# Kernel tuning notes

Hardware: AMD Instinct MI355X
Metric: run time of the kernel (lower is better)

## Reference

```python
import jax, jax.numpy as jnp
import numpy as np

EPS = 1e-12  # torch F.normalize eps

N, C, H, W = 64, 512, 40, 40
K = 64  # num_clusters


def setup_inputs() -> dict:
    key = jax.random.key(0)
    k1, k2, k3 = jax.random.split(key, 3)
    x = jax.random.normal(k1, (N, C, H, W), dtype=jnp.float32)
    conv_w = jax.random.normal(k2, (K, C, 1, 1), dtype=jnp.float32) * 0.05
    centroids = jax.random.uniform(k3, (K, C), dtype=jnp.float32)
    return {"x": x, "conv_w": conv_w, "centroids": centroids}


def _l2norm(v, axis):
    return v / jnp.maximum(jnp.sqrt(jnp.sum(v * v, axis=axis, keepdims=True)), EPS)


def reference(x, conv_w, centroids):
    n, c = x.shape[:2]
    k = conv_w.shape[0]
    # descriptor-wise L2 normalization over channels
    xn = _l2norm(x, axis=1)
    xf = xn.reshape(n, c, -1)  # [N, C, P]
    # 1x1 conv (no bias, vladv2=False) == per-pixel matmul with [K, C]
    logits = jnp.einsum('kc,ncp->nkp', conv_w.reshape(k, c), xf)
    a = jax.nn.softmax(logits, axis=1)  # soft assignment over clusters
    # VLAD: sum_p a[n,k,p] * (x[n,:,p] - centroid[k])  (weights are all-ones)
    vlad = jnp.einsum('nkp,ncp->nkc', a, xf) - a.sum(axis=-1)[:, :, None] * centroids[None]
    # intra-normalization over C, flatten, global L2 norm
    vlad = _l2norm(vlad, axis=2).reshape(n, -1)
    vlad = _l2norm(vlad, axis=1)
    return vlad
```

## Files before the change

kernel.cpp:

```cpp
#include <hip/hip_runtime.h>
#include <math.h>

#define EPSF 1e-12f


typedef short bf16x8 __attribute__((ext_vector_type(8)));
typedef float f32x4  __attribute__((ext_vector_type(4)));

__device__ __forceinline__ ushort f2b(float x) {
    unsigned u = __float_as_uint(x);
    return (ushort)((u + 0x7fffu + ((u >> 16) & 1u)) >> 16);
}

__global__ __launch_bounds__(256) void k0_wb(const float* __restrict__ W,
                                             ushort* __restrict__ Wb) {
    int i = blockIdx.x * 256 + threadIdx.x;
    if (i < 64 * 512) Wb[i] = f2b(W[i]);
}

__global__ __launch_bounds__(256) void k2g_gemm1(const float* __restrict__ x,
                                                 const ushort* __restrict__ Wb,
                                                 ushort* __restrict__ a_t,
                                                 float* __restrict__ asum) {
    const int n = blockIdx.y;
    const int p0 = blockIdx.x * 64;
    const int wv = threadIdx.x >> 6, lane = threadIdx.x & 63;
    const int q = lane >> 4, l15 = lane & 15;
    const int pw = p0 + wv * 16;

    const float* xq = x + (size_t)n * 512 * 1600 + (size_t)q * 8 * 1600 + pw + l15;
    const ushort* brow = Wb + l15 * 512 + q * 8;

    f32x4 acc[4] = {};
    float ssp = 0.f;
    for (int kc = 0; kc < 16; kc++) {
        float fv[8];
        #pragma unroll
        for (int j = 0; j < 8; j++) fv[j] = xq[(size_t)(kc * 32 + j) * 1600];
        bf16x8 af;
        #pragma unroll
        for (int j = 0; j < 8; j++) {
            ssp = fmaf(fv[j], fv[j], ssp);
            af[j] = (short)f2b(fv[j]);
        }
        #pragma unroll
        for (int nt = 0; nt < 4; nt++) {
            bf16x8 bw = *(const bf16x8*)(brow + nt * 16 * 512 + kc * 32);
            acc[nt] = __builtin_amdgcn_mfma_f32_16x16x32_bf16(af, bw, acc[nt], 0, 0, 0);
        }
    }
    ssp += __shfl_xor(ssp, 16, 64);
    ssp += __shfl_xor(ssp, 32, 64);
    float rn_l = 1.f / fmaxf(sqrtf(ssp), EPSF);
    float rnv[4];
    #pragma unroll
    for (int r = 0; r < 4; r++) rnv[r] = __shfl(rn_l, q * 4 + r, 64);

    float v[4][4];
    float mx[4] = {-3.4e38f, -3.4e38f, -3.4e38f, -3.4e38f};
    #pragma unroll
    for (int nt = 0; nt < 4; nt++)
        #pragma unroll
        for (int r = 0; r < 4; r++) {
            v[nt][r] = acc[nt][r] * rnv[r];
            mx[r] = fmaxf(mx[r], v[nt][r]);
        }
    #pragma unroll
    for (int s = 1; s <= 8; s <<= 1)
        #pragma unroll
        for (int r = 0; r < 4; r++) mx[r] = fmaxf(mx[r], __shfl_xor(mx[r], s, 64));
    float sm[4] = {0.f, 0.f, 0.f, 0.f};
    #pragma unroll
    for (int nt = 0; nt < 4; nt++)
        #pragma unroll
        for (int r = 0; r < 4; r++) { v[nt][r] = __expf(v[nt][r] - mx[r]); sm[r] += v[nt][r]; }
    #pragma unroll
    for (int s = 1; s <= 8; s <<= 1)
        #pragma unroll
        for (int r = 0; r < 4; r++) sm[r] += __shfl_xor(sm[r], s, 64);
    float inv[4];
    #pragma unroll
    for (int r = 0; r < 4; r++) inv[r] = 1.f / sm[r];
    #pragma unroll
    for (int nt = 0; nt < 4; nt++)
        #pragma unroll
        for (int r = 0; r < 4; r++) v[nt][r] *= inv[r];

    #pragma unroll
    for (int nt = 0; nt < 4; nt++) {
        float t = v[nt][0] + v[nt][1] + v[nt][2] + v[nt][3];
        t += __shfl_xor(t, 16, 64);
        t += __shfl_xor(t, 32, 64);
        if (lane < 16) atomicAdd(&asum[n * 64 + nt * 16 + lane], t);
    }

    __shared__ ushort abuf[4][64 * 24];
    #pragma unroll
    for (int nt = 0; nt < 4; nt++)
        #pragma unroll
        for (int r = 0; r < 4; r++)
            abuf[wv][(nt * 16 + l15) * 24 + q * 4 + r] = f2b(v[nt][r] * rnv[r]);
    __syncthreads();
    ushort* dst = a_t + ((size_t)n * 64 + lane) * 1600 + pw;
    const ushort* srcl = &abuf[wv][lane * 24];
    *(uint4*)(dst)     = *(const uint4*)(srcl);
    *(uint4*)(dst + 8) = *(const uint4*)(srcl + 8);
}

__global__ __launch_bounds__(256) void k3_gemm2(const ushort* __restrict__ a_t,
                                                const float* __restrict__ x,
                                                float* __restrict__ out) {
    const int n = blockIdx.y;
    const int c0 = blockIdx.x * 256;
    const int p0 = blockIdx.z * 320;
    const int wv = threadIdx.x >> 6, lane = threadIdx.x & 63;
    const int q = lane >> 4, l15 = lane & 15;
    const int cw = c0 + wv * 64;

    const ushort* abase = a_t + ((size_t)n * 64 + l15) * 1600 + p0 + q * 8;
    const float*  xbase = x + ((size_t)n * 512 + cw + l15) * 1600 + p0 + q * 8;

    f32x4 acc[4][4] = {};
    for (int pc = 0; pc < 320; pc += 32) {
        bf16x8 af[4];
        #pragma unroll
        for (int mt = 0; mt < 4; mt++)
            af[mt] = *(const bf16x8*)(abase + (size_t)mt * 16 * 1600 + pc);
        bf16x8 bf[4];
        #pragma unroll
        for (int nt = 0; nt < 4; nt++) {
            const float* xr = xbase + (size_t)nt * 16 * 1600 + pc;
            float4 f0 = *(const float4*)(xr);
            float4 f1 = *(const float4*)(xr + 4);
            bf16x8 b;
            b[0] = (short)f2b(f0.x); b[1] = (short)f2b(f0.y);
            b[2] = (short)f2b(f0.z); b[3] = (short)f2b(f0.w);
            b[4] = (short)f2b(f1.x); b[5] = (short)f2b(f1.y);
            b[6] = (short)f2b(f1.z); b[7] = (short)f2b(f1.w);
            bf[nt] = b;
        }
        #pragma unroll
        for (int mt = 0; mt < 4; mt++)
            #pragma unroll
            for (int nt = 0; nt < 4; nt++)
                acc[mt][nt] = __builtin_amdgcn_mfma_f32_16x16x32_bf16(af[mt], bf[nt], acc[mt][nt], 0, 0, 0);
    }
    float* ob = out + (size_t)n * 32768 + cw + l15;
    #pragma unroll
    for (int mt = 0; mt < 4; mt++)
        #pragma unroll
        for (int nt = 0; nt < 4; nt++)
            #pragma unroll
            for (int r = 0; r < 4; r++)
                atomicAdd(ob + (mt * 16 + q * 4 + r) * 512 + nt * 16, acc[mt][nt][r]);
}

__global__ __launch_bounds__(256) void k4a_rownorm(const float* __restrict__ vraw,
                                                   const float* __restrict__ asum,
                                                   const float* __restrict__ cent,
                                                   float* __restrict__ rn2) {
    int row  = blockIdx.x * 4 + (threadIdx.x >> 6);
    int lane = threadIdx.x & 63;
    int k = row & 63;
    const float4* vp = (const float4*)(vraw + (size_t)row * 512 + lane * 8);
    const float4* cp = (const float4*)(cent + k * 512 + lane * 8);
    float as = asum[row];
    float4 v0 = vp[0], v1 = vp[1], c0 = cp[0], c1 = cp[1];
    float s = 0.f, t;
    t = v0.x - as * c0.x; s = fmaf(t, t, s);
    t = v0.y - as * c0.y; s = fmaf(t, t, s);
    t = v0.z - as * c0.z; s = fmaf(t, t, s);
    t = v0.w - as * c0.w; s = fmaf(t, t, s);
    t = v1.x - as * c1.x; s = fmaf(t, t, s);
    t = v1.y - as * c1.y; s = fmaf(t, t, s);
    t = v1.z - as * c1.z; s = fmaf(t, t, s);
    t = v1.w - as * c1.w; s = fmaf(t, t, s);
    #pragma unroll
    for (int off = 32; off > 0; off >>= 1) s += __shfl_down(s, off, 64);
    if (lane == 0) rn2[row] = s;
}

__global__ __launch_bounds__(64) void k4b_gn(const float* __restrict__ rn2,
                                             float* __restrict__ gn) {
    int n = blockIdx.x, k = threadIdx.x;
    float t = rn2[n * 64 + k];
    float d = fmaxf(sqrtf(t), EPSF);
    float r = t / (d * d);
    #pragma unroll
    for (int off = 32; off > 0; off >>= 1) r += __shfl_down(r, off, 64);
    if (k == 0) gn[n] = fmaxf(sqrtf(r), EPSF);
}

__global__ __launch_bounds__(256) void k4c_final(float* __restrict__ vout,
                                                 const float* __restrict__ asum,
                                                 const float* __restrict__ cent,
                                                 const float* __restrict__ rn2,
                                                 const float* __restrict__ gn) {
    int gid = blockIdx.x * 256 + threadIdx.x;
    int idx4 = gid * 4;
    int row = idx4 >> 9;
    int n = row >> 6, k = row & 63, c = idx4 & 511;
    float4 v  = *(const float4*)(vout + idx4);
    float4 cv = *(const float4*)(cent + k * 512 + c);
    float as = asum[row];
    float inv = 1.f / (fmaxf(sqrtf(rn2[row]), EPSF) * gn[n]);
    v.x = (v.x - as * cv.x) * inv;
    v.y = (v.y - as * cv.y) * inv;
    v.z = (v.z - as * cv.z) * inv;
    v.w = (v.w - as * cv.w) * inv;
    *(float4*)(vout + idx4) = v;
}

extern "C" void kernel_launch(void* const* d_in, const int* in_sizes, int n_in,
                              void* d_out, int out_size, void* d_ws, size_t ws_size,
                              hipStream_t stream) {
    const float* x    = (const float*)d_in[0];
    const float* W    = (const float*)d_in[1];
    const float* cent = (const float*)d_in[2];
    float* out = (float*)d_out;
    char* ws = (char*)d_ws;

    ushort* a_t  = (ushort*)(ws + 0);
    ushort* Wb   = (ushort*)(ws + 13107200);
    float*  asum = (float*)(ws + 13172736);
    float*  rn2  = (float*)(ws + 13189120);
    float*  gn   = (float*)(ws + 13205504);

    hipMemsetAsync(asum, 0, 64 * 64 * sizeof(float), stream);
    hipMemsetAsync(d_out, 0, (size_t)out_size * sizeof(float), stream);

    hipLaunchKernelGGL(k0_wb,       dim3(128),      dim3(256), 0, stream, W, Wb);
    hipLaunchKernelGGL(k2g_gemm1,   dim3(25, 64),   dim3(256), 0, stream, x, Wb, a_t, asum);
    hipLaunchKernelGGL(k3_gemm2,    dim3(2, 64, 5), dim3(256), 0, stream, a_t, x, out);
    hipLaunchKernelGGL(k4a_rownorm, dim3(1024),     dim3(256), 0, stream, out, asum, cent, rn2);
    hipLaunchKernelGGL(k4b_gn,      dim3(64),       dim3(64),  0, stream, rn2, gn);
    hipLaunchKernelGGL(k4c_final,   dim3(2048),     dim3(256), 0, stream, out, asum, cent, rn2, gn);
}
```

Before: 401.2 us.

## Fuse assignment GEMM, softmax and VLAD aggregation GEMM into one kernel

Merges the logits/softmax kernel and the aggregation kernel into a single kernel. Each block walks five 32-pixel chunks, computes the soft assignment into shared memory and immediately multiplies it against x. This drops the bf16 assignment round-trip through global memory and one launch, and accumulates asum in registers before a single atomic. In exchange, grid parallelism drops to 640 blocks, the accumulator tile is larger (register pressure under launch_bounds 256,2), there are several block syncs per chunk, and x is read twice within the block.

```diff
diff --git a/kernel.cpp b/kernel.cpp
--- a/kernel.cpp
+++ b/kernel.cpp
@@ -18,141 +18,148 @@
     if (i < 64 * 512) Wb[i] = f2b(W[i]);
 }
 
-__global__ __launch_bounds__(256) void k2g_gemm1(const float* __restrict__ x,
-                                                 const ushort* __restrict__ Wb,
-                                                 ushort* __restrict__ a_t,
-                                                 float* __restrict__ asum) {
-    const int n = blockIdx.y;
-    const int p0 = blockIdx.x * 64;
-    const int wv = threadIdx.x >> 6, lane = threadIdx.x & 63;
+#define ASTR 40
+
+__global__ __launch_bounds__(256, 2) void k_fused2(const float* __restrict__ x,
+                                                   const ushort* __restrict__ Wb,
+                                                   float* __restrict__ out,
+                                                   float* __restrict__ asum) {
+    const int n  = blockIdx.y;
+    const int pg = blockIdx.x;
+    const int w = threadIdx.x >> 6, lane = threadIdx.x & 63;
     const int q = lane >> 4, l15 = lane & 15;
-    const int pw = p0 + wv * 16;
-
-    const float* xq = x + (size_t)n * 512 * 1600 + (size_t)q * 8 * 1600 + pw + l15;
-    const ushort* brow = Wb + l15 * 512 + q * 8;
-
-    f32x4 acc[4] = {};
-    float ssp = 0.f;
-    for (int kc = 0; kc < 16; kc++) {
-        float fv[8];
-        #pragma unroll
-        for (int j = 0; j < 8; j++) fv[j] = xq[(size_t)(kc * 32 + j) * 1600];
-        bf16x8 af;
-        #pragma unroll
-        for (int j = 0; j < 8; j++) {
-            ssp = fmaf(fv[j], fv[j], ssp);
-            af[j] = (short)f2b(fv[j]);
-        }
-        #pragma unroll
-        for (int nt = 0; nt < 4; nt++) {
-            bf16x8 bw = *(const bf16x8*)(brow + nt * 16 * 512 + kc * 32);
-            acc[nt] = __builtin_amdgcn_mfma_f32_16x16x32_bf16(af, bw, acc[nt], 0, 0, 0);
-        }
-    }
-    ssp += __shfl_xor(ssp, 16, 64);
-    ssp += __shfl_xor(ssp, 32, 64);
-    float rn_l = 1.f / fmaxf(sqrtf(ssp), EPSF);
-    float rnv[4];
-    #pragma unroll
-    for (int r = 0; r < 4; r++) rnv[r] = __shfl(rn_l, q * 4 + r, 64);
-
-    float v[4][4];
-    float mx[4] = {-3.4e38f, -3.4e38f, -3.4e38f, -3.4e38f};
-    #pragma unroll
-    for (int nt = 0; nt < 4; nt++)
-        #pragma unroll
-        for (int r = 0; r < 4; r++) {
-            v[nt][r] = acc[nt][r] * rnv[r];
-            mx[r] = fmaxf(mx[r], v[nt][r]);
-        }
-    #pragma unroll
-    for (int s = 1; s <= 8; s <<= 1)
-        #pragma unroll
-        for (int r = 0; r < 4; r++) mx[r] = fmaxf(mx[r], __shfl_xor(mx[r], s, 64));
-    float sm[4] = {0.f, 0.f, 0.f, 0.f};
-    #pragma unroll
-    for (int nt = 0; nt < 4; nt++)
-        #pragma unroll
-        for (int r = 0; r < 4; r++) { v[nt][r] = __expf(v[nt][r] - mx[r]); sm[r] += v[nt][r]; }
-    #pragma unroll
-    for (int s = 1; s <= 8; s <<= 1)
-        #pragma unroll
-        for (int r = 0; r < 4; r++) sm[r] += __shfl_xor(sm[r], s, 64);
-    float inv[4];
-    #pragma unroll
-    for (int r = 0; r < 4; r++) inv[r] = 1.f / sm[r];
-    #pragma unroll
-    for (int nt = 0; nt < 4; nt++)
-        #pragma unroll
-        for (int r = 0; r < 4; r++) v[nt][r] *= inv[r];
-
-    #pragma unroll
-    for (int nt = 0; nt < 4; nt++) {
-        float t = v[nt][0] + v[nt][1] + v[nt][2] + v[nt][3];
-        t += __shfl_xor(t, 16, 64);
-        t += __shfl_xor(t, 32, 64);
-        if (lane < 16) atomicAdd(&asum[n * 64 + nt * 16 + lane], t);
-    }
-
-    __shared__ ushort abuf[4][64 * 24];
-    #pragma unroll
-    for (int nt = 0; nt < 4; nt++)
+    const int pt = w & 1;
+    const int kh = w >> 1;
+
+    __shared__ float  smx[2][2][16];
+    __shared__ float  ssm[2][2][16];
+    __shared__ ushort as_[64 * ASTR] __attribute__((aligned(16)));
+
+    f32x4 acc2[4][8] = {};
+    float asum_acc[2] = {0.f, 0.f};
+
+    for (int ch = 0; ch < 5; ch++) {
+        const int pch = pg * 160 + ch * 32;
+        const int pw  = pch + pt * 16;
+
+        const float* xq = x + (size_t)n * 512 * 1600 + (size_t)q * 8 * 1600 + pw + l15;
+        const ushort* brow = Wb + (kh * 32 + l15) * 512 + q * 8;
+        f32x4 acc1[2] = {};
+        float ssp = 0.f;
+        for (int kc = 0; kc < 16; kc++) {
+            float fv[8];
+            #pragma unroll
+            for (int j = 0; j < 8; j++) fv[j] = xq[(size_t)(kc * 32 + j) * 1600];
+            bf16x8 af;
+            #pragma unroll
+            for (int j = 0; j < 8; j++) {
+                ssp = fmaf(fv[j], fv[j], ssp);
+                af[j] = (short)f2b(fv[j]);
+            }
+            #pragma unroll
+            for (int nt = 0; nt < 2; nt++) {
+                bf16x8 bw = *(const bf16x8*)(brow + nt * 16 * 512 + kc * 32);
+                acc1[nt] = __builtin_amdgcn_mfma_f32_16x16x32_bf16(af, bw, acc1[nt], 0, 0, 0);
+            }
+        }
+        ssp += __shfl_xor(ssp, 16, 64);
+        ssp += __shfl_xor(ssp, 32, 64);
+        float rn_l = 1.f / fmaxf(sqrtf(ssp), EPSF);
+        float rnv[4];
+        #pragma unroll
+        for (int r = 0; r < 4; r++) rnv[r] = __shfl(rn_l, q * 4 + r, 64);
+
+        float v[2][4];
+        float mx[4] = {-3.4e38f, -3.4e38f, -3.4e38f, -3.4e38f};
+        #pragma unroll
+        for (int nt = 0; nt < 2; nt++)
+            #pragma unroll
+            for (int r = 0; r < 4; r++) {
+                v[nt][r] = acc1[nt][r] * rnv[r];
+                mx[r] = fmaxf(mx[r], v[nt][r]);
+            }
+        #pragma unroll
+        for (int s = 1; s <= 8; s <<= 1)
+            #pragma unroll
+            for (int r = 0; r < 4; r++) mx[r] = fmaxf(mx[r], __shfl_xor(mx[r], s, 64));
+        if (l15 == 0) {
+            #pragma unroll
+            for (int r = 0; r < 4; r++) smx[kh][pt][q * 4 + r] = mx[r];
+        }
+        __syncthreads();
+        float gmx[4];
+        #pragma unroll
+        for (int r = 0; r < 4; r++) gmx[r] = fmaxf(smx[0][pt][q * 4 + r], smx[1][pt][q * 4 + r]);
+        float sm[4] = {0.f, 0.f, 0.f, 0.f};
+        #pragma unroll
+        for (int nt = 0; nt < 2; nt++)
+            #pragma unroll
+            for (int r = 0; r < 4; r++) { v[nt][r] = __expf(v[nt][r] - gmx[r]); sm[r] += v[nt][r]; }
+        #pragma unroll
+        for (int s = 1; s <= 8; s <<= 1)
+            #pragma unroll
+            for (int r = 0; r < 4; r++) sm[r] += __shfl_xor(sm[r], s, 64);
+        if (l15 == 0) {
+            #pragma unroll
+            for (int r = 0; r < 4; r++) ssm[kh][pt][q * 4 + r] = sm[r];
+        }
+        __syncthreads();
+        float inv[4];
         #pragma unroll
         for (int r = 0; r < 4; r++)
-            abuf[wv][(nt * 16 + l15) * 24 + q * 4 + r] = f2b(v[nt][r] * rnv[r]);
-    __syncthreads();
-    ushort* dst = a_t + ((size_t)n * 64 + lane) * 1600 + pw;
-    const ushort* srcl = &abuf[wv][lane * 24];
-    *(uint4*)(dst)     = *(const uint4*)(srcl);
-    *(uint4*)(dst + 8) = *(const uint4*)(srcl + 8);
-}
-
-__global__ __launch_bounds__(256) void k3_gemm2(const ushort* __restrict__ a_t,
-                                                const float* __restrict__ x,
-                                                float* __restrict__ out) {
-    const int n = blockIdx.y;
-    const int c0 = blockIdx.x * 256;
-    const int p0 = blockIdx.z * 320;
-    const int wv = threadIdx.x >> 6, lane = threadIdx.x & 63;
-    const int q = lane >> 4, l15 = lane & 15;
-    const int cw = c0 + wv * 64;
-
-    const ushort* abase = a_t + ((size_t)n * 64 + l15) * 1600 + p0 + q * 8;
-    const float*  xbase = x + ((size_t)n * 512 + cw + l15) * 1600 + p0 + q * 8;
-
-    f32x4 acc[4][4] = {};
-    for (int pc = 0; pc < 320; pc += 32) {
-        bf16x8 af[4];
+            inv[r] = 1.f / (ssm[0][pt][q * 4 + r] + ssm[1][pt][q * 4 + r]);
+
+        #pragma unroll
+        for (int nt = 0; nt < 2; nt++) {
+            float t = v[nt][0] * inv[0] + v[nt][1] * inv[1] + v[nt][2] * inv[2] + v[nt][3] * inv[3];
+            t += __shfl_xor(t, 16, 64);
+            t += __shfl_xor(t, 32, 64);
+            asum_acc[nt] += t;
+        }
+
+        #pragma unroll
+        for (int nt = 0; nt < 2; nt++)
+            #pragma unroll
+            for (int r = 0; r < 4; r++)
+                as_[(kh * 32 + nt * 16 + l15) * ASTR + pt * 16 + q * 4 + r] =
+                    f2b(v[nt][r] * inv[r] * rnv[r]);
+        __syncthreads();
+
+        const int cw = w * 128;
+        bf16x8 afr[4];
         #pragma unroll
         for (int mt = 0; mt < 4; mt++)
-            af[mt] = *(const bf16x8*)(abase + (size_t)mt * 16 * 1600 + pc);
-        bf16x8 bf[4];
-        #pragma unroll
-        for (int nt = 0; nt < 4; nt++) {
-            const float* xr = xbase + (size_t)nt * 16 * 1600 + pc;
-            float4 f0 = *(const float4*)(xr);
-            float4 f1 = *(const float4*)(xr + 4);
+            afr[mt] = *(const bf16x8*)(as_ + (mt * 16 + l15) * ASTR + q * 8);
+        #pragma unroll
+        for (int ct = 0; ct < 8; ct++) {
+            const float* xb = x + ((size_t)(n * 512 + cw + ct * 16 + l15)) * 1600 + pch + q * 8;
+            float4 f0 = *(const float4*)(xb);
+            float4 f1 = *(const float4*)(xb + 4);
             bf16x8 b;
             b[0] = (short)f2b(f0.x); b[1] = (short)f2b(f0.y);
             b[2] = (short)f2b(f0.z); b[3] = (short)f2b(f0.w);
             b[4] = (short)f2b(f1.x); b[5] = (short)f2b(f1.y);
             b[6] = (short)f2b(f1.z); b[7] = (short)f2b(f1.w);
-            bf[nt] = b;
-        }
-        #pragma unroll
-        for (int mt = 0; mt < 4; mt++)
-            #pragma unroll
-            for (int nt = 0; nt < 4; nt++)
-                acc[mt][nt] = __builtin_amdgcn_mfma_f32_16x16x32_bf16(af[mt], bf[nt], acc[mt][nt], 0, 0, 0);
+            #pragma unroll
+            for (int mt = 0; mt < 4; mt++)
+                acc2[mt][ct] = __builtin_amdgcn_mfma_f32_16x16x32_bf16(afr[mt], b, acc2[mt][ct], 0, 0, 0);
+        }
+        __syncthreads();
     }
-    float* ob = out + (size_t)n * 32768 + cw + l15;
+
+    if (lane < 16) {
+        #pragma unroll
+        for (int nt = 0; nt < 2; nt++)
+            atomicAdd(&asum[n * 64 + kh * 32 + nt * 16 + lane], asum_acc[nt]);
+    }
+    float* ob = out + (size_t)n * 32768 + w * 128 + l15;
     #pragma unroll
     for (int mt = 0; mt < 4; mt++)
         #pragma unroll
-        for (int nt = 0; nt < 4; nt++)
+        for (int ct = 0; ct < 8; ct++)
             #pragma unroll
             for (int r = 0; r < 4; r++)
-                atomicAdd(ob + (mt * 16 + q * 4 + r) * 512 + nt * 16, acc[mt][nt][r]);
+                atomicAdd(ob + (mt * 16 + q * 4 + r) * 512 + ct * 16, acc2[mt][ct][r]);
 }
 
 __global__ __launch_bounds__(256) void k4a_rownorm(const float* __restrict__ vraw,
@@ -220,19 +227,17 @@
     float* out = (float*)d_out;
     char* ws = (char*)d_ws;
 
-    ushort* a_t  = (ushort*)(ws + 0);
-    ushort* Wb   = (ushort*)(ws + 13107200);
-    float*  asum = (float*)(ws + 13172736);
-    float*  rn2  = (float*)(ws + 13189120);
-    float*  gn   = (float*)(ws + 13205504);
+    ushort* Wb   = (ushort*)(ws + 0);
+    float*  asum = (float*)(ws + 65536);
+    float*  rn2  = (float*)(ws + 81920);
+    float*  gn   = (float*)(ws + 98304);
 
     hipMemsetAsync(asum, 0, 64 * 64 * sizeof(float), stream);
     hipMemsetAsync(d_out, 0, (size_t)out_size * sizeof(float), stream);
 
-    hipLaunchKernelGGL(k0_wb,       dim3(128),      dim3(256), 0, stream, W, Wb);
-    hipLaunchKernelGGL(k2g_gemm1,   dim3(25, 64),   dim3(256), 0, stream, x, Wb, a_t, asum);
-    hipLaunchKernelGGL(k3_gemm2,    dim3(2, 64, 5), dim3(256), 0, stream, a_t, x, out);
-    hipLaunchKernelGGL(k4a_rownorm, dim3(1024),     dim3(256), 0, stream, out, asum, cent, rn2);
-    hipLaunchKernelGGL(k4b_gn,      dim3(64),       dim3(64),  0, stream, rn2, gn);
-    hipLaunchKernelGGL(k4c_final,   dim3(2048),     dim3(256), 0, stream, out, asum, cent, rn2, gn);
-}
+    hipLaunchKernelGGL(k0_wb,       dim3(128),    dim3(256), 0, stream, W, Wb);
+    hipLaunchKernelGGL(k_fused2,    dim3(10, 64), dim3(256), 0, stream, x, Wb, out, asum);
+    hipLaunchKernelGGL(k4a_rownorm, dim3(1024),   dim3(256), 0, stream, out, asum, cent, rn2);
+    hipLaunchKernelGGL(k4b_gn,      dim3(64),     dim3(64),  0, stream, rn2, gn);
+    hipLaunchKernelGGL(k4c_final,   dim3(2048),   dim3(256), 0, stream, out, asum, cent, rn2, gn);
+}
```

Measured after the change: 481.2 us. +20.0%, slower.
